# Optimization experiments

Hardware: AMD Instinct MI355X
Metric: run time of the kernel (lower is better)

Reference implementation:

```python
import jax, jax.numpy as jnp
import numpy as np

B, L, D, F = 8, 1024, 256, 11
TEMP = D ** 0.5
LN_EPS = 1e-6


def setup_inputs() -> dict:
    key = jax.random.key(0)
    ks = jax.random.split(key, 14)
    mk = lambda k, s: jax.random.normal(k, s, dtype=jnp.float32)
    return {
        "q": mk(ks[0], (B, L, D)),
        "k": mk(ks[1], (B, L, D)),
        "v": mk(ks[2], (B, L, D)),
        "x": jax.random.uniform(ks[3], (B, L, F), dtype=jnp.float32),
        "inputs_lengths": jax.random.randint(ks[4], (B,), 512, L + 1),
        "w_qs": mk(ks[5], (D, D)) * 0.05,
        "w_ks": mk(ks[6], (D, D)) * 0.05,
        "w_vs": mk(ks[7], (D, D)) * 0.05,
        "w_qs2": mk(ks[8], (D, D)) * 0.05,
        "w_ks2": mk(ks[9], (D, D)) * 0.05,
        "w_fc": mk(ks[10], (D, D)) * 0.05,
        "feature_importance": mk(ks[11], (F,)) * 0.1,
        "ln_gamma": jnp.ones((D,), jnp.float32),
        "ln_beta": jnp.zeros((D,), jnp.float32),
    }


def reference(q, k, v, x, w_qs, w_ks, w_vs, w_qs2, w_ks2, w_fc,
              feature_importance, ln_gamma, ln_beta, inputs_lengths):
    lin = lambda a, w: jnp.einsum('bli,oi->blo', a, w)  # torch Linear: y = x W^T
    qp = lin(q, w_qs)
    kp = lin(k, w_ks)
    vp = lin(v, w_vs)
    q2 = lin(q, w_qs2)
    k2 = lin(k, w_ks2)

    # key-position validity mask [B, L]
    key_mask = jnp.arange(L)[None, :] < inputs_lengths[:, None]

    # FeatureSim: pairwise L1 feature distances weighted by feature_importance
    fd = jnp.abs(x[:, :, None, :] - x[:, None, :, :])           # [B,L,L,F]
    fa = jnp.einsum('bijf,f->bij', fd, feature_importance)      # [B,L,L]
    fa = jnp.where(key_mask[:, None, :], fa, -jnp.inf)          # pad_masking
    fa = jax.nn.softmax(fa, axis=-1)
    fa = jnp.nan_to_num(fa)                                     # nan -> 0 for fully-masked rows

    # dual-score attention with tanh activation (no row normalization)
    attn = jnp.einsum('bid,bjd->bij', qp / TEMP, kp)
    q2f = jnp.einsum('bij,bjd->bid', fa, q2)
    k2f = jnp.einsum('bij,bjd->bid', fa, k2)
    attn = attn + jnp.einsum('bid,bjd->bij', q2f / TEMP, k2f)
    zm = key_mask[:, None, :]
    attn = jnp.where(zm, attn, 0.0)                             # pad_zero_masking
    attn = jnp.tanh(attn)
    attn = jnp.where(zm, attn, 0.0)                             # pad_zero_masking (tanh(0)=0, kept for fidelity)

    out = jnp.einsum('bij,bjd->bid', attn, vp)
    out = lin(out, w_fc) + q                                    # dropout is identity at eval
    mu = jnp.mean(out, axis=-1, keepdims=True)
    var = jnp.var(out, axis=-1, keepdims=True)
    out = (out - mu) / jnp.sqrt(var + LN_EPS) * ln_gamma + ln_beta
    return (out, attn)
```

## Files before the change

### kernel.cpp

```cpp
#include <hip/hip_runtime.h>
#include <hip/hip_bf16.h>
#include <math.h>

typedef __hip_bfloat16 bf16;
typedef __bf16 bf16x8 __attribute__((ext_vector_type(8)));
typedef float  f32x4  __attribute__((ext_vector_type(4)));

#define NB 8
#define SL 1024
#define DD 256
#define NF 11
#define RPB 8

#define AS_G __attribute__((address_space(1)))
#define AS_L __attribute__((address_space(3)))

__device__ __forceinline__ bf16x8 ldfrag(const bf16* p) {
  return *reinterpret_cast<const bf16x8*>(p);
}
__device__ __forceinline__ bf16x8 ldfrag(const float* p) {
  const float4 a = *reinterpret_cast<const float4*>(p);
  const float4 b = *reinterpret_cast<const float4*>(p + 4);
  bf16x8 r;
  r[0] = (__bf16)a.x; r[1] = (__bf16)a.y; r[2] = (__bf16)a.z; r[3] = (__bf16)a.w;
  r[4] = (__bf16)b.x; r[5] = (__bf16)b.y; r[6] = (__bf16)b.z; r[7] = (__bf16)b.w;
  return r;
}
__device__ __forceinline__ unsigned short us(float f) {
  bf16 h = __float2bfloat16(f);
  return *reinterpret_cast<unsigned short*>(&h);
}
__device__ __forceinline__ float tanh_fast(float x) {
  return 1.f - 2.f / (__expf(2.f * x) + 1.f);
}

template<int R>
__device__ __forceinline__ void stage_t(const float* __restrict__ g, int ld,
                                        bf16* __restrict__ s, int tid) {
#pragma unroll
  for (int it = 0; it < R / 32; ++it) {
    const int cid = it * 256 + tid;
    const int row = cid >> 3, c16 = cid & 7;
    bf16x8 v = ldfrag(g + (size_t)row * ld + c16 * 8);
    *reinterpret_cast<bf16x8*>(s + row * 64 + ((c16 ^ (row & 7)) << 3)) = v;
  }
}
template<int R>
__device__ __forceinline__ void stage_t(const bf16* __restrict__ g, int ld,
                                        bf16* __restrict__ s, int tid) {
  const int wbase = tid & ~63;
#pragma unroll
  for (int it = 0; it < R / 32; ++it) {
    const int cid = it * 256 + tid;
    const int row = cid >> 3, sc = cid & 7;
    const int c16 = sc ^ (row & 7);
    const bf16* src = g + (size_t)row * ld + c16 * 8;
    bf16* dst = s + (size_t)(it * 256 + wbase) * 8;
    __builtin_amdgcn_global_load_lds((const AS_G void*)src, (AS_L void*)dst, 16, 0, 0);
  }
}

__device__ __forceinline__ void compute_64x128(const bf16* __restrict__ sA,
                                               const bf16* __restrict__ sB,
                                               int lane, int wave, f32x4 acc[4][2]) {
  const int n15 = lane & 15, quad = lane >> 4;
  const int wn = wave * 32;
#pragma unroll
  for (int kc = 0; kc < 2; ++kc) {
    const int c16 = kc * 4 + quad;
    bf16x8 aF[4], bF[2];
#pragma unroll
    for (int t = 0; t < 4; ++t) {
      const int ra = t * 16 + n15;
      aF[t] = *reinterpret_cast<const bf16x8*>(sA + ra * 64 + ((c16 ^ (ra & 7)) << 3));
    }
#pragma unroll
    for (int t = 0; t < 2; ++t) {
      const int rb = wn + t * 16 + n15;
      bF[t] = *reinterpret_cast<const bf16x8*>(sB + rb * 64 + ((c16 ^ (rb & 7)) << 3));
    }
#pragma unroll
    for (int ti = 0; ti < 4; ++ti)
#pragma unroll
      for (int tj = 0; tj < 2; ++tj)
        acc[ti][tj] = __builtin_amdgcn_mfma_f32_16x16x32_bf16(aF[ti], bF[tj], acc[ti][tj], 0, 0, 0);
  }
}

template<typename TA, typename TB>
__device__ __forceinline__ void gemm_64x128(const TA* __restrict__ A, int lda,
                                            const TB* __restrict__ B, int ldb, int K,
                                            bf16* s, int tid, f32x4 acc[4][2]) {
  const int lane = tid & 63, wave = tid >> 6;
  bf16* sA = s;
  bf16* sB = s + 4096;
  for (int k0 = 0; k0 < K; k0 += 64) {
    stage_t<64>(A + k0, lda, sA, tid);
    stage_t<128>(B + k0, ldb, sB, tid);
    __syncthreads();
    compute_64x128(sA, sB, lane, wave, acc);
    __syncthreads();
  }
}

__device__ __forceinline__ float wred_sum(float v) {
#pragma unroll
  for (int o = 32; o > 0; o >>= 1) v += __shfl_xor(v, o, 64);
  return v;
}

__global__ __launch_bounds__(256) void k_prep(const float* __restrict__ q,
                                              const float* __restrict__ k,
                                              const float* __restrict__ v,
                                              const float* __restrict__ wfc,
                                              const float* __restrict__ wvs,
                                              bf16* __restrict__ cq,
                                              bf16* __restrict__ ck,
                                              bf16* __restrict__ cv,
                                              float* __restrict__ Wc)
{
  const int bid = blockIdx.x, tid = threadIdx.x;
  if (bid < 1536) {
    const int which = bid >> 9, sub = bid & 511;
    const float* src = (which == 0) ? q : (which == 1) ? k : v;
    bf16* dst = (which == 0) ? cq : (which == 1) ? ck : cv;
    const size_t base = (size_t)sub * 4096;
#pragma unroll
    for (int it = 0; it < 4; ++it) {
      const size_t off = base + (size_t)(it * 256 + tid) * 4;
      const float4 a = *reinterpret_cast<const float4*>(src + off);
      ushort4 pk = make_ushort4(us(a.x), us(a.y), us(a.z), us(a.w));
      *reinterpret_cast<ushort4*>(dst + off) = pk;
    }
  } else {
    const int o = bid - 1536, m = tid;
    const float* fr = wfc + (size_t)o * DD;
    float acc = 0.f;
#pragma unroll 8
    for (int i = 0; i < DD; ++i)
      acc += fr[i] * wvs[(size_t)i * DD + m];
    Wc[(size_t)o * DD + m] = acc;
  }
}

__global__ __launch_bounds__(256) void k_proj(
    const bf16* __restrict__ cq, const bf16* __restrict__ ck, const bf16* __restrict__ cv,
    const float* __restrict__ wqs, const float* __restrict__ wks, const float* __restrict__ Wc,
    const float* __restrict__ wqs2, const float* __restrict__ wks2,
    bf16* __restrict__ qq, bf16* __restrict__ kk,
    bf16* __restrict__ vpwt, bf16* __restrict__ q2t, bf16* __restrict__ k2t)
{
  __shared__ bf16 smem[12288];
  const int tid = threadIdx.x, lane = tid & 63, wave = tid >> 6;
  const int z = blockIdx.z;
  const bf16*  A = (z == 2) ? cv : ((z == 1 || z == 4) ? ck : cq);
  const float* W = (z == 0) ? wqs : (z == 1) ? wks : (z == 2) ? Wc : (z == 3) ? wqs2 : wks2;
  const int rowBase = blockIdx.x * 64;
  const int colBase = blockIdx.y * 128;
  f32x4 acc[4][2] = {};
  gemm_64x128(A + (size_t)rowBase * DD, DD, W + (size_t)colBase * DD, DD, DD, smem, tid, acc);
  const int n15 = lane & 15, quad = lane >> 4;
  const int wn = wave * 32;
  if (z <= 1) {
    bf16* O = (z == 0) ? qq : kk;
#pragma unroll
    for (int ti = 0; ti < 4; ++ti)
#pragma unroll
      for (int tj = 0; tj < 2; ++tj)
#pragma unroll
        for (int r = 0; r < 4; ++r) {
          int row = rowBase + ti * 16 + quad * 4 + r;
          int col = colBase + wn + tj * 16 + n15;
          O[(size_t)row * 512 + col] = __float2bfloat16(acc[ti][tj][r]);
        }
  } else {
    bf16* O = (z == 2) ? vpwt : (z == 3) ? q2t : k2t;
    const int bb = rowBase >> 10, rowInB = rowBase & 1023;
#pragma unroll
    for (int ti = 0; ti < 4; ++ti)
#pragma unroll
      for (int tj = 0; tj < 2; ++tj) {
        int l0  = rowInB + ti * 16 + quad * 4;
        int col = colBase + wn + tj * 16 + n15;
        ushort4 pk = make_ushort4(us(acc[ti][tj][0]), us(acc[ti][tj][1]),
                                  us(acc[ti][tj][2]), us(acc[ti][tj][3]));
        *reinterpret_cast<ushort4*>(&O[((size_t)bb * DD + col) * SL + l0]) = pk;
      }
  }
}

__global__ __launch_bounds__(256) void k_fa(const float* __restrict__ x,
                                            const float* __restrict__ fi_g,
                                            const int* __restrict__ lens,
                                            bf16* __restrict__ fa)
{
  __shared__ __align__(16) float sx[SL * NF];
  __shared__ float sredS[4][RPB];
  const int tid = threadIdx.x, wave = tid >> 6;
  const int b  = blockIdx.x >> 7;
  const int i0 = (blockIdx.x & 127) * RPB;
  {
    const float4* src = reinterpret_cast<const float4*>(x + (size_t)b * SL * NF);
    float4* dst = reinterpret_cast<float4*>(sx);
#pragma unroll
    for (int it = 0; it < 11; ++it) dst[it * 256 + tid] = src[it * 256 + tid];
  }
  float fiv[NF];
#pragma unroll
  for (int f = 0; f < NF; ++f) fiv[f] = fi_g[f];
  const int len = lens[b];
  __syncthreads();
  float xi[RPB][NF];
#pragma unroll
  for (int i = 0; i < RPB; ++i)
#pragma unroll
    for (int f = 0; f < NF; ++f) xi[i][f] = sx[(i0 + i) * NF + f];
  float e[RPB][4];
  float ps[RPB];
#pragma unroll
  for (int i = 0; i < RPB; ++i) ps[i] = 0.f;
#pragma unroll
  for (int t = 0; t < 4; ++t) {
    const int j = tid + t * 256;
    const bool valid = (t < 2) || (j < len);
    float xj[NF];
#pragma unroll
    for (int f = 0; f < NF; ++f) xj[f] = sx[j * NF + f];
#pragma unroll
    for (int i = 0; i < RPB; ++i) {
      float a = 0.f;
#pragma unroll
      for (int f = 0; f < NF; ++f) a += fabsf(xi[i][f] - xj[f]) * fiv[f];
      float ev = valid ? __expf(a) : 0.f;
      e[i][t] = ev;
      ps[i] += ev;
    }
  }
#pragma unroll
  for (int i = 0; i < RPB; ++i) {
    float wsv = wred_sum(ps[i]);
    if ((tid & 63) == 0) sredS[wave][i] = wsv;
  }
  __syncthreads();
  bf16* out = fa + (size_t)b * SL * SL + (size_t)i0 * SL;
#pragma unroll
  for (int i = 0; i < RPB; ++i) {
    const float inv = 1.f / (sredS[0][i] + sredS[1][i] + sredS[2][i] + sredS[3][i]);
#pragma unroll
    for (int t = 0; t < 4; ++t)
      out[(size_t)i * SL + tid + t * 256] = __float2bfloat16(e[i][t] * inv);
  }
}

__global__ __launch_bounds__(256) void k_famul(const bf16* __restrict__ fa,
                                               const bf16* __restrict__ q2t,
                                               const bf16* __restrict__ k2t,
                                               bf16* __restrict__ qq,
                                               bf16* __restrict__ kk)
{
  __shared__ bf16 smem[12288];
  const int tid = threadIdx.x, lane = tid & 63, wave = tid >> 6;
  const int flat = blockIdx.x + 16 * blockIdx.y + 32 * blockIdx.z;
  const int lid  = (flat & 7) * 64 + (flat >> 3);
  const int bx = lid & 15, by = (lid >> 4) & 1, bz = lid >> 5;
  const int b = bz >> 1, which = bz & 1;
  const int iBase = bx * 64, dBase = by * 128;
  const bf16* A  = fa + (size_t)b * SL * SL + (size_t)iBase * SL;
  const bf16* Bm = (which ? k2t : q2t) + (size_t)b * DD * SL + (size_t)dBase * SL;
  f32x4 acc[4][2] = {};
  gemm_64x128(A, SL, Bm, SL, SL, smem, tid, acc);
  bf16* O = (which ? kk : qq) + (size_t)b * SL * 512 + 256;
  const int n15 = lane & 15, quad = lane >> 4;
  const int wn = wave * 32;
#pragma unroll
  for (int ti = 0; ti < 4; ++ti)
#pragma unroll
    for (int tj = 0; tj < 2; ++tj)
#pragma unroll
      for (int r = 0; r < 4; ++r)
        O[(size_t)(iBase + ti * 16 + quad * 4 + r) * 512 +
          dBase + wn + tj * 16 + n15] = __float2bfloat16(acc[ti][tj][r]);
}

__global__ __launch_bounds__(256) void k_attn(const bf16* __restrict__ qq,
                                              const bf16* __restrict__ kk,
                                              const int* __restrict__ lens,
                                              float* __restrict__ attn_f32,
                                              bf16* __restrict__ attn_b16)
{
  __shared__ bf16 smem[12288];
  const int tid = threadIdx.x, lane = tid & 63, wave = tid >> 6;
  const int flat = blockIdx.x + 16 * blockIdx.y + 128 * blockIdx.z;
  const int lid  = (flat & 7) * 128 + (flat >> 3);
  const int bx = lid & 15, by = (lid >> 4) & 7, bz = lid >> 7;
  const int b = bz;
  const int iBase = bx * 64, jBase = by * 128;
  f32x4 acc[4][2] = {};
  gemm_64x128(qq + ((size_t)b * SL + iBase) * 512, 512,
              kk + ((size_t)b * SL + jBase) * 512, 512, 512, smem, tid, acc);
  const int len = lens[b];
  const int n15 = lane & 15, quad = lane >> 4;
  const int wn = wave * 32;
#pragma unroll
  for (int ti = 0; ti < 4; ++ti)
#pragma unroll
    for (int tj = 0; tj < 2; ++tj)
#pragma unroll
      for (int r = 0; r < 4; ++r) {
        int i = iBase + ti * 16 + quad * 4 + r;
        int j = jBase + wn + tj * 16 + n15;
        float vv = (j < len) ? tanh_fast(acc[ti][tj][r] * (1.f / 16.f)) : 0.f;
        size_t idx = (size_t)b * SL * SL + (size_t)i * SL + j;
        attn_f32[idx] = vv;
        attn_b16[idx] = __float2bfloat16(vv);
      }
}

__global__ __launch_bounds__(256) void k_av(const bf16* __restrict__ attn,
                                            const bf16* __restrict__ vpwt,
                                            const float* __restrict__ qres,
                                            float* __restrict__ fcout)
{
  __shared__ bf16 smem[12288];
  const int tid = threadIdx.x, lane = tid & 63, wave = tid >> 6;
  const int flat = blockIdx.x + 16 * blockIdx.y + 32 * blockIdx.z;
  const int lid  = (flat & 7) * 32 + (flat >> 3);
  const int bx = lid & 15, by = (lid >> 4) & 1, bz = lid >> 5;
  const int b = bz;
  const int iBase = bx * 64, dBase = by * 128;
  f32x4 acc[4][2] = {};
  gemm_64x128(attn + (size_t)b * SL * SL + (size_t)iBase * SL, SL,
              vpwt + (size_t)b * DD * SL + (size_t)dBase * SL, SL, SL, smem, tid, acc);
  const int n15 = lane & 15, quad = lane >> 4;
  const int wn = wave * 32;
#pragma unroll
  for (int ti = 0; ti < 4; ++ti)
#pragma unroll
    for (int tj = 0; tj < 2; ++tj)
#pragma unroll
      for (int r = 0; r < 4; ++r) {
        size_t row = (size_t)b * SL + iBase + ti * 16 + quad * 4 + r;
        int col = dBase + wn + tj * 16 + n15;
        fcout[row * DD + col] = acc[ti][tj][r] + qres[row * DD + col];
      }
}

__global__ __launch_bounds__(256) void k_ln(const float* __restrict__ fcout,
                                            const float* __restrict__ gam,
                                            const float* __restrict__ bet,
                                            float* __restrict__ outp)
{
  __shared__ float r1[4], r2[4];
  const int r = blockIdx.x, tid = threadIdx.x;
  const float v = fcout[(size_t)r * DD + tid];
  float s = wred_sum(v), ss = wred_sum(v * v);
  if ((tid & 63) == 0) { r1[tid >> 6] = s; r2[tid >> 6] = ss; }
  __syncthreads();
  s  = r1[0] + r1[1] + r1[2] + r1[3];
  ss = r2[0] + r2[1] + r2[2] + r2[3];
  const float mean = s * (1.f / DD);
  const float var  = ss * (1.f / DD) - mean * mean;
  float y = (v - mean) * rsqrtf(var + 1e-6f);
  y = y * gam[tid] + bet[tid];
  outp[(size_t)r * DD + tid] = y;
}

extern "C" void kernel_launch(void* const* d_in, const int* in_sizes, int n_in,
                              void* d_out, int out_size, void* d_ws, size_t ws_size,
                              hipStream_t stream)
{
  const float* q    = (const float*)d_in[0];
  const float* k    = (const float*)d_in[1];
  const float* v    = (const float*)d_in[2];
  const float* x    = (const float*)d_in[3];
  const int*  lens  = (const int*)d_in[4];
  const float* wqs  = (const float*)d_in[5];
  const float* wks  = (const float*)d_in[6];
  const float* wvs  = (const float*)d_in[7];
  const float* wqs2 = (const float*)d_in[8];
  const float* wks2 = (const float*)d_in[9];
  const float* wfc  = (const float*)d_in[10];
  const float* fi   = (const float*)d_in[11];
  const float* gam  = (const float*)d_in[12];
  const float* bet  = (const float*)d_in[13];

  char* w = (char*)d_ws;
  const size_t MB = 1u << 20;
  const size_t KB = 1u << 10;
  bf16* qq    = (bf16*)(w + 0 * MB);
  bf16* kk    = (bf16*)(w + 8 * MB);
  bf16* vpwt  = (bf16*)(w + 16 * MB);
  bf16* q2t   = (bf16*)(w + 20 * MB);
  bf16* k2t   = (bf16*)(w + 24 * MB);
  bf16* cq    = (bf16*)(w + 28 * MB);
  bf16* ck    = (bf16*)(w + 32 * MB);
  bf16* cv    = (bf16*)(w + 36 * MB);
  float* Wc   = (float*)(w + 40 * MB);
  bf16* fa    = (bf16*)(w + 28 * MB);
  bf16* attn_b16 = fa;
  float* fcout = (float*)(w + 0 * MB);

  float* outp  = (float*)d_out;
  float* attnp = outp + (size_t)NB * SL * DD;
  (void)KB; (void)wvs;

  dim3 blk(256);
  hipLaunchKernelGGL(k_prep,  dim3(1792),      blk, 0, stream, q, k, v, wfc, wvs,
                     cq, ck, cv, Wc);
  hipLaunchKernelGGL(k_proj,  dim3(128, 2, 5), blk, 0, stream,
                     cq, ck, cv, wqs, wks, Wc, wqs2, wks2, qq, kk, vpwt, q2t, k2t);
  hipLaunchKernelGGL(k_fa,    dim3(NB * 128),  blk, 0, stream, x, fi, lens, fa);
  hipLaunchKernelGGL(k_famul, dim3(16, 2, 16), blk, 0, stream, fa, q2t, k2t, qq, kk);
  hipLaunchKernelGGL(k_attn,  dim3(16, 8, 8),  blk, 0, stream,
                     qq, kk, lens, attnp, attn_b16);
  hipLaunchKernelGGL(k_av,    dim3(16, 2, 8),  blk, 0, stream, attn_b16, vpwt, q, fcout);
  hipLaunchKernelGGL(k_ln,    dim3(NB * SL),   blk, 0, stream, fcout, gam, bet, outp);
}
```

Baseline: 209.4 us.

## Use double-buffered 128x128 GEMM tiles and skip padded key ranges

Grows the shared GEMM tile from 64x128 to 128x128 (a 2x2 wave layout with 4x4 MFMA accumulators) and double-buffers the LDS stage, so the load of the next K slice overlaps compute and each iteration needs only one barrier. The famul and av GEMMs now stop their K loop at the rounded-up sequence length. The attn kernel writes zeros directly for column tiles that lie entirely beyond the length, skipping the GEMM there. In exchange it uses more LDS and registers and launches fewer blocks, which lowers occupancy and the block count on the GPU.

```diff
diff --git a/kernel.cpp b/kernel.cpp
--- a/kernel.cpp
+++ b/kernel.cpp
@@ -60,46 +60,49 @@
   }
 }
 
-__device__ __forceinline__ void compute_64x128(const bf16* __restrict__ sA,
-                                               const bf16* __restrict__ sB,
-                                               int lane, int wave, f32x4 acc[4][2]) {
+__device__ __forceinline__ void compute_128x128(const bf16* __restrict__ sA,
+                                                const bf16* __restrict__ sB,
+                                                int lane, int wave, f32x4 acc[4][4]) {
   const int n15 = lane & 15, quad = lane >> 4;
-  const int wn = wave * 32;
+  const int wr = (wave >> 1) << 6, wc = (wave & 1) << 6;
 #pragma unroll
   for (int kc = 0; kc < 2; ++kc) {
     const int c16 = kc * 4 + quad;
-    bf16x8 aF[4], bF[2];
+    bf16x8 aF[4], bF[4];
 #pragma unroll
     for (int t = 0; t < 4; ++t) {
-      const int ra = t * 16 + n15;
+      const int ra = wr + t * 16 + n15;
       aF[t] = *reinterpret_cast<const bf16x8*>(sA + ra * 64 + ((c16 ^ (ra & 7)) << 3));
-    }
-#pragma unroll
-    for (int t = 0; t < 2; ++t) {
-      const int rb = wn + t * 16 + n15;
+      const int rb = wc + t * 16 + n15;
       bF[t] = *reinterpret_cast<const bf16x8*>(sB + rb * 64 + ((c16 ^ (rb & 7)) << 3));
     }
 #pragma unroll
     for (int ti = 0; ti < 4; ++ti)
 #pragma unroll
-      for (int tj = 0; tj < 2; ++tj)
+      for (int tj = 0; tj < 4; ++tj)
         acc[ti][tj] = __builtin_amdgcn_mfma_f32_16x16x32_bf16(aF[ti], bF[tj], acc[ti][tj], 0, 0, 0);
   }
 }
 
 template<typename TA, typename TB>
-__device__ __forceinline__ void gemm_64x128(const TA* __restrict__ A, int lda,
-                                            const TB* __restrict__ B, int ldb, int K,
-                                            bf16* s, int tid, f32x4 acc[4][2]) {
+__device__ __forceinline__ void gemm_128x128(const TA* __restrict__ A, int lda,
+                                             const TB* __restrict__ B, int ldb, int K,
+                                             bf16* s, int tid, f32x4 acc[4][4]) {
   const int lane = tid & 63, wave = tid >> 6;
-  bf16* sA = s;
-  bf16* sB = s + 4096;
+  stage_t<128>(A, lda, s, tid);
+  stage_t<128>(B, ldb, s + 8192, tid);
+  int cur = 0;
+  __syncthreads();
   for (int k0 = 0; k0 < K; k0 += 64) {
-    stage_t<64>(A + k0, lda, sA, tid);
-    stage_t<128>(B + k0, ldb, sB, tid);
+    bf16* sc0 = s + cur * 16384;
+    if (k0 + 64 < K) {
+      bf16* sn = s + (cur ^ 1) * 16384;
+      stage_t<128>(A + k0 + 64, lda, sn, tid);
+      stage_t<128>(B + k0 + 64, ldb, sn + 8192, tid);
+    }
+    compute_128x128(sc0, sc0 + 8192, lane, wave, acc);
     __syncthreads();
-    compute_64x128(sA, sB, lane, wave, acc);
-    __syncthreads();
+    cur ^= 1;
   }
 }
 
@@ -150,27 +153,27 @@
     bf16* __restrict__ qq, bf16* __restrict__ kk,
     bf16* __restrict__ vpwt, bf16* __restrict__ q2t, bf16* __restrict__ k2t)
 {
-  __shared__ bf16 smem[12288];
+  __shared__ bf16 smem[32768];
   const int tid = threadIdx.x, lane = tid & 63, wave = tid >> 6;
   const int z = blockIdx.z;
   const bf16*  A = (z == 2) ? cv : ((z == 1 || z == 4) ? ck : cq);
   const float* W = (z == 0) ? wqs : (z == 1) ? wks : (z == 2) ? Wc : (z == 3) ? wqs2 : wks2;
-  const int rowBase = blockIdx.x * 64;
+  const int rowBase = blockIdx.x * 128;
   const int colBase = blockIdx.y * 128;
-  f32x4 acc[4][2] = {};
-  gemm_64x128(A + (size_t)rowBase * DD, DD, W + (size_t)colBase * DD, DD, DD, smem, tid, acc);
+  f32x4 acc[4][4] = {};
+  gemm_128x128(A + (size_t)rowBase * DD, DD, W + (size_t)colBase * DD, DD, DD, smem, tid, acc);
   const int n15 = lane & 15, quad = lane >> 4;
-  const int wn = wave * 32;
+  const int wr = (wave >> 1) << 6, wc = (wave & 1) << 6;
   if (z <= 1) {
     bf16* O = (z == 0) ? qq : kk;
 #pragma unroll
     for (int ti = 0; ti < 4; ++ti)
 #pragma unroll
-      for (int tj = 0; tj < 2; ++tj)
+      for (int tj = 0; tj < 4; ++tj)
 #pragma unroll
         for (int r = 0; r < 4; ++r) {
-          int row = rowBase + ti * 16 + quad * 4 + r;
-          int col = colBase + wn + tj * 16 + n15;
+          int row = rowBase + wr + ti * 16 + quad * 4 + r;
+          int col = colBase + wc + tj * 16 + n15;
           O[(size_t)row * 512 + col] = __float2bfloat16(acc[ti][tj][r]);
         }
   } else {
@@ -179,9 +182,9 @@
 #pragma unroll
     for (int ti = 0; ti < 4; ++ti)
 #pragma unroll
-      for (int tj = 0; tj < 2; ++tj) {
-        int l0  = rowInB + ti * 16 + quad * 4;
-        int col = colBase + wn + tj * 16 + n15;
+      for (int tj = 0; tj < 4; ++tj) {
+        int l0  = rowInB + wr + ti * 16 + quad * 4;
+        int col = colBase + wc + tj * 16 + n15;
         ushort4 pk = make_ushort4(us(acc[ti][tj][0]), us(acc[ti][tj][1]),
                                   us(acc[ti][tj][2]), us(acc[ti][tj][3]));
         *reinterpret_cast<ushort4*>(&O[((size_t)bb * DD + col) * SL + l0]) = pk;
@@ -255,31 +258,33 @@
 __global__ __launch_bounds__(256) void k_famul(const bf16* __restrict__ fa,
                                                const bf16* __restrict__ q2t,
                                                const bf16* __restrict__ k2t,
+                                               const int* __restrict__ lens,
                                                bf16* __restrict__ qq,
                                                bf16* __restrict__ kk)
 {
-  __shared__ bf16 smem[12288];
+  __shared__ bf16 smem[32768];
   const int tid = threadIdx.x, lane = tid & 63, wave = tid >> 6;
-  const int flat = blockIdx.x + 16 * blockIdx.y + 32 * blockIdx.z;
-  const int lid  = (flat & 7) * 64 + (flat >> 3);
-  const int bx = lid & 15, by = (lid >> 4) & 1, bz = lid >> 5;
+  const int flat = blockIdx.x + 8 * blockIdx.y + 16 * blockIdx.z;
+  const int lid  = (flat & 7) * 32 + (flat >> 3);
+  const int bx = lid & 7, by = (lid >> 3) & 1, bz = lid >> 4;
   const int b = bz >> 1, which = bz & 1;
-  const int iBase = bx * 64, dBase = by * 128;
+  const int iBase = bx * 128, dBase = by * 128;
+  const int Keff = (lens[b] + 63) & ~63;
   const bf16* A  = fa + (size_t)b * SL * SL + (size_t)iBase * SL;
   const bf16* Bm = (which ? k2t : q2t) + (size_t)b * DD * SL + (size_t)dBase * SL;
-  f32x4 acc[4][2] = {};
-  gemm_64x128(A, SL, Bm, SL, SL, smem, tid, acc);
+  f32x4 acc[4][4] = {};
+  gemm_128x128(A, SL, Bm, SL, Keff, smem, tid, acc);
   bf16* O = (which ? kk : qq) + (size_t)b * SL * 512 + 256;
   const int n15 = lane & 15, quad = lane >> 4;
-  const int wn = wave * 32;
+  const int wr = (wave >> 1) << 6, wc = (wave & 1) << 6;
 #pragma unroll
   for (int ti = 0; ti < 4; ++ti)
 #pragma unroll
-    for (int tj = 0; tj < 2; ++tj)
+    for (int tj = 0; tj < 4; ++tj)
 #pragma unroll
       for (int r = 0; r < 4; ++r)
-        O[(size_t)(iBase + ti * 16 + quad * 4 + r) * 512 +
-          dBase + wn + tj * 16 + n15] = __float2bfloat16(acc[ti][tj][r]);
+        O[(size_t)(iBase + wr + ti * 16 + quad * 4 + r) * 512 +
+          dBase + wc + tj * 16 + n15] = __float2bfloat16(acc[ti][tj][r]);
 }
 
 __global__ __launch_bounds__(256) void k_attn(const bf16* __restrict__ qq,
@@ -288,27 +293,39 @@
                                               float* __restrict__ attn_f32,
                                               bf16* __restrict__ attn_b16)
 {
-  __shared__ bf16 smem[12288];
+  __shared__ bf16 smem[32768];
   const int tid = threadIdx.x, lane = tid & 63, wave = tid >> 6;
-  const int flat = blockIdx.x + 16 * blockIdx.y + 128 * blockIdx.z;
-  const int lid  = (flat & 7) * 128 + (flat >> 3);
-  const int bx = lid & 15, by = (lid >> 4) & 7, bz = lid >> 7;
+  const int flat = blockIdx.x + 8 * blockIdx.y + 64 * blockIdx.z;
+  const int lid  = (flat & 7) * 64 + (flat >> 3);
+  const int bx = lid & 7, by = (lid >> 3) & 7, bz = lid >> 6;
   const int b = bz;
-  const int iBase = bx * 64, jBase = by * 128;
-  f32x4 acc[4][2] = {};
-  gemm_64x128(qq + ((size_t)b * SL + iBase) * 512, 512,
-              kk + ((size_t)b * SL + jBase) * 512, 512, 512, smem, tid, acc);
+  const int iBase = bx * 128, jBase = by * 128;
   const int len = lens[b];
+  if (jBase >= len) {
+    const int r = tid >> 1, ch = (tid & 1) * 64;
+    float* pf = attn_f32 + (size_t)b * SL * SL + (size_t)(iBase + r) * SL + jBase + ch;
+    bf16*  pb = attn_b16 + (size_t)b * SL * SL + (size_t)(iBase + r) * SL + jBase + ch;
+    const float4 z4 = make_float4(0.f, 0.f, 0.f, 0.f);
+    const uint4  zb = make_uint4(0u, 0u, 0u, 0u);
+#pragma unroll
+    for (int i = 0; i < 16; ++i) *reinterpret_cast<float4*>(pf + i * 4) = z4;
+#pragma unroll
+    for (int i = 0; i < 8; ++i)  *reinterpret_cast<uint4*>(pb + i * 8) = zb;
+    return;
+  }
+  f32x4 acc[4][4] = {};
+  gemm_128x128(qq + ((size_t)b * SL + iBase) * 512, 512,
+               kk + ((size_t)b * SL + jBase) * 512, 512, 512, smem, tid, acc);
   const int n15 = lane & 15, quad = lane >> 4;
-  const int wn = wave * 32;
+  const int wr = (wave >> 1) << 6, wc = (wave & 1) << 6;
 #pragma unroll
   for (int ti = 0; ti < 4; ++ti)
 #pragma unroll
-    for (int tj = 0; tj < 2; ++tj)
+    for (int tj = 0; tj < 4; ++tj)
 #pragma unroll
       for (int r = 0; r < 4; ++r) {
-        int i = iBase + ti * 16 + quad * 4 + r;
-        int j = jBase + wn + tj * 16 + n15;
+        int i = iBase + wr + ti * 16 + quad * 4 + r;
+        int j = jBase + wc + tj * 16 + n15;
         float vv = (j < len) ? tanh_fast(acc[ti][tj][r] * (1.f / 16.f)) : 0.f;
         size_t idx = (size_t)b * SL * SL + (size_t)i * SL + j;
         attn_f32[idx] = vv;
@@ -319,28 +336,30 @@
 __global__ __launch_bounds__(256) void k_av(const bf16* __restrict__ attn,
                                             const bf16* __restrict__ vpwt,
                                             const float* __restrict__ qres,
+                                            const int* __restrict__ lens,
                                             float* __restrict__ fcout)
 {
-  __shared__ bf16 smem[12288];
+  __shared__ bf16 smem[32768];
   const int tid = threadIdx.x, lane = tid & 63, wave = tid >> 6;
-  const int flat = blockIdx.x + 16 * blockIdx.y + 32 * blockIdx.z;
-  const int lid  = (flat & 7) * 32 + (flat >> 3);
-  const int bx = lid & 15, by = (lid >> 4) & 1, bz = lid >> 5;
+  const int flat = blockIdx.x + 8 * blockIdx.y + 16 * blockIdx.z;
+  const int lid  = (flat & 7) * 16 + (flat >> 3);
+  const int bx = lid & 7, by = (lid >> 3) & 1, bz = lid >> 4;
   const int b = bz;
-  const int iBase = bx * 64, dBase = by * 128;
-  f32x4 acc[4][2] = {};
-  gemm_64x128(attn + (size_t)b * SL * SL + (size_t)iBase * SL, SL,
-              vpwt + (size_t)b * DD * SL + (size_t)dBase * SL, SL, SL, smem, tid, acc);
+  const int iBase = bx * 128, dBase = by * 128;
+  const int Keff = (lens[b] + 63) & ~63;
+  f32x4 acc[4][4] = {};
+  gemm_128x128(attn + (size_t)b * SL * SL + (size_t)iBase * SL, SL,
+               vpwt + (size_t)b * DD * SL + (size_t)dBase * SL, SL, Keff, smem, tid, acc);
   const int n15 = lane & 15, quad = lane >> 4;
-  const int wn = wave * 32;
+  const int wr = (wave >> 1) << 6, wc = (wave & 1) << 6;
 #pragma unroll
   for (int ti = 0; ti < 4; ++ti)
 #pragma unroll
-    for (int tj = 0; tj < 2; ++tj)
+    for (int tj = 0; tj < 4; ++tj)
 #pragma unroll
       for (int r = 0; r < 4; ++r) {
-        size_t row = (size_t)b * SL + iBase + ti * 16 + quad * 4 + r;
-        int col = dBase + wn + tj * 16 + n15;
+        size_t row = (size_t)b * SL + iBase + wr + ti * 16 + quad * 4 + r;
+        int col = dBase + wc + tj * 16 + n15;
         fcout[row * DD + col] = acc[ti][tj][r] + qres[row * DD + col];
       }
 }
@@ -407,12 +426,12 @@
   dim3 blk(256);
   hipLaunchKernelGGL(k_prep,  dim3(1792),      blk, 0, stream, q, k, v, wfc, wvs,
                      cq, ck, cv, Wc);
-  hipLaunchKernelGGL(k_proj,  dim3(128, 2, 5), blk, 0, stream,
+  hipLaunchKernelGGL(k_proj,  dim3(64, 2, 5),  blk, 0, stream,
                      cq, ck, cv, wqs, wks, Wc, wqs2, wks2, qq, kk, vpwt, q2t, k2t);
   hipLaunchKernelGGL(k_fa,    dim3(NB * 128),  blk, 0, stream, x, fi, lens, fa);
-  hipLaunchKernelGGL(k_famul, dim3(16, 2, 16), blk, 0, stream, fa, q2t, k2t, qq, kk);
-  hipLaunchKernelGGL(k_attn,  dim3(16, 8, 8),  blk, 0, stream,
+  hipLaunchKernelGGL(k_famul, dim3(8, 2, 16),  blk, 0, stream, fa, q2t, k2t, lens, qq, kk);
+  hipLaunchKernelGGL(k_attn,  dim3(8, 8, 8),   blk, 0, stream,
                      qq, kk, lens, attnp, attn_b16);
-  hipLaunchKernelGGL(k_av,    dim3(16, 2, 8),  blk, 0, stream, attn_b16, vpwt, q, fcout);
+  hipLaunchKernelGGL(k_av,    dim3(8, 2, 8),   blk, 0, stream, attn_b16, vpwt, q, lens, fcout);
   hipLaunchKernelGGL(k_ln,    dim3(NB * SL),   blk, 0, stream, fcout, gam, bet, outp);
 }
```

Measured after the change: 200.6 us. -4.2%, faster.
